# Kernel tuning notes

Hardware: AMD Instinct MI355X
Metric: run time of the kernel (lower is better)

Reference implementation:

```python
import jax, jax.numpy as jnp
import numpy as np

HEAD_DIM = 256
HIDDEN = 1536
INTERMEDIATE = 6144
NUM_KV_HEADS = 1
NUM_Q_HEADS = 8
SCALE = HEAD_DIM ** (-0.5)
PAST_LEN = 8191


def setup_inputs() -> dict:
    key = jax.random.key(0)
    ks = jax.random.split(key, 20)
    def lin(ki, fan_in, fan_out):
        # torch nn.Linear init: U(-1/sqrt(fan_in), 1/sqrt(fan_in)); stored (in, out) for x @ W
        bound = 1.0 / np.sqrt(fan_in)
        W = jax.random.uniform(ki, (fan_in, fan_out), jnp.float32, -bound, bound)
        b = jax.random.uniform(jax.random.fold_in(ki, 1), (fan_out,), jnp.float32, -bound, bound)
        return W, b
    Wq, bq = lin(ks[0], HIDDEN, NUM_Q_HEADS * HEAD_DIM)
    Wk, bk = lin(ks[1], HIDDEN, NUM_KV_HEADS * HEAD_DIM)
    Wv, bv = lin(ks[2], HIDDEN, NUM_KV_HEADS * HEAD_DIM)
    Wo, bo = lin(ks[3], NUM_Q_HEADS * HEAD_DIM, HIDDEN)
    Wg, bg = lin(ks[4], HIDDEN, INTERMEDIATE)
    Wu, bu = lin(ks[5], HIDDEN, INTERMEDIATE)
    Wd, bd = lin(ks[6], INTERMEDIATE, HIDDEN)
    x = jax.random.normal(ks[7], (1, 1, HIDDEN), jnp.float32)
    k_past = jax.random.normal(ks[8], (1, NUM_KV_HEADS, PAST_LEN, HEAD_DIM), jnp.float32)
    v_past = jax.random.normal(ks[9], (1, NUM_KV_HEADS, PAST_LEN, HEAD_DIM), jnp.float32)
    return dict(x=x, k_past=k_past, v_past=v_past,
                Wq=Wq, bq=bq, Wk=Wk, bk=bk, Wv=Wv, bv=bv, Wo=Wo, bo=bo,
                Wg=Wg, bg=bg, Wu=Wu, bu=bu, Wd=Wd, bd=bd)


def reference(x, k_past, v_past, Wq, bq, Wk, bk, Wv, bv, Wo, bo, Wg, bg, Wu, bu, Wd, bd):
    residual = x
    # projections; q: (1, Hq, 1, D), k/v: (1, Hkv, 1, D)
    q = (x @ Wq + bq).reshape(1, 1, NUM_Q_HEADS, HEAD_DIM).transpose(0, 2, 1, 3)
    k = (x @ Wk + bk).reshape(1, 1, NUM_KV_HEADS, HEAD_DIM).transpose(0, 2, 1, 3)
    v = (x @ Wv + bv).reshape(1, 1, NUM_KV_HEADS, HEAD_DIM).transpose(0, 2, 1, 3)
    k_full = jnp.concatenate([k_past, k], axis=2)  # (1, Hkv, S, D)
    v_full = jnp.concatenate([v_past, v], axis=2)
    # GQA: broadcast the single KV head across 8 Q heads (no materialized repeat)
    scores = jnp.einsum('bhqd,bksd->bhqs', q, k_full) * SCALE  # (1, Hq, 1, S)
    attn = jax.nn.softmax(scores, axis=-1)
    out = jnp.einsum('bhqs,bksd->bhqd', attn, v_full)  # (1, Hq, 1, D)
    out = out.transpose(0, 2, 1, 3).reshape(1, 1, NUM_Q_HEADS * HEAD_DIM)
    out = out @ Wo + bo
    x = residual + out
    # MLP: GELU(gate) * up -> down (exact erf GELU, matching torch nn.GELU default)
    ffn = (jax.nn.gelu(x @ Wg + bg, approximate=False) * (x @ Wu + bu)) @ Wd + bd
    return x + ffn
```

## Files before the change

### kernel.cpp

```cpp
#include <hip/hip_runtime.h>
#include <hip/hip_bf16.h>
#include <math.h>

#define PAST 8191
#define SCALEF 0.0625f

using bf = __hip_bfloat16;

__device__ __forceinline__ float bf2f(unsigned short u) {
    return __uint_as_float(((unsigned)u) << 16);
}
__device__ __forceinline__ void unpack8(uint4 r, float* f) {
    f[0] = __uint_as_float(r.x << 16);
    f[1] = __uint_as_float(r.x & 0xffff0000u);
    f[2] = __uint_as_float(r.y << 16);
    f[3] = __uint_as_float(r.y & 0xffff0000u);
    f[4] = __uint_as_float(r.z << 16);
    f[5] = __uint_as_float(r.z & 0xffff0000u);
    f[6] = __uint_as_float(r.w << 16);
    f[7] = __uint_as_float(r.w & 0xffff0000u);
}

template<bool BF16>
__device__ __forceinline__ void load8(const void* W, size_t off, float* f) {
    if constexpr (BF16) {
        uint4 r = *reinterpret_cast<const uint4*>((const unsigned short*)W + off);
        unpack8(r, f);
    } else {
        const float* p = (const float*)W + off;
        float4 a = *reinterpret_cast<const float4*>(p);
        float4 b = *reinterpret_cast<const float4*>(p + 4);
        f[0]=a.x; f[1]=a.y; f[2]=a.z; f[3]=a.w;
        f[4]=b.x; f[5]=b.y; f[6]=b.z; f[7]=b.w;
    }
}
template<bool BF16>
__device__ __forceinline__ void load4(const void* P, size_t off, float* f) {
    if constexpr (BF16) {
        uint2 r = *reinterpret_cast<const uint2*>((const unsigned short*)P + off);
        f[0] = __uint_as_float(r.x << 16); f[1] = __uint_as_float(r.x & 0xffff0000u);
        f[2] = __uint_as_float(r.y << 16); f[3] = __uint_as_float(r.y & 0xffff0000u);
    } else {
        float4 a = *reinterpret_cast<const float4*>((const float*)P + off);
        f[0]=a.x; f[1]=a.y; f[2]=a.z; f[3]=a.w;
    }
}
template<bool BF16>
__device__ __forceinline__ float load1(const void* P, int i) {
    if constexpr (BF16) return bf2f(((const unsigned short*)P)[i]);
    else return ((const float*)P)[i];
}

__global__ __launch_bounds__(256) void probe_kernel(const unsigned int* __restrict__ xw,
                                                    int* __restrict__ flag) {
    __shared__ int cnt;
    if (threadIdx.x == 0) cnt = 0;
    __syncthreads();
    int ok = 0;
    for (int i = threadIdx.x; i < 768; i += 256) {
        unsigned e = (xw[i] >> 7) & 0xff;
        if (e >= 96 && e <= 142) ok++;
    }
    atomicAdd(&cnt, ok);
    __syncthreads();
    if (threadIdx.x == 0) *flag = (cnt > 500) ? 1 : 0;
}

template<bool BF16>
__device__ void qkv_body(const void* x, const void* Wq, const void* bq,
                         const void* Wk, const void* bk, const void* Wv, const void* bv,
                         float* qkv) {
    __shared__ float xs[64];
    int tid = threadIdx.x;
    int i0 = blockIdx.y * 64;
    xs[tid] = load1<BF16>(x, i0 + tid);
    __syncthreads();
    int j = blockIdx.x * 512 + tid * 8;
    const void* W; const void* bias; int stride, jl;
    if (j < 2048)      { W = Wq; bias = bq; stride = 2048; jl = j; }
    else if (j < 2304) { W = Wk; bias = bk; stride = 256;  jl = j - 2048; }
    else               { W = Wv; bias = bv; stride = 256;  jl = j - 2304; }
    float acc[8] = {0,0,0,0,0,0,0,0};
    #pragma unroll 4
    for (int i = 0; i < 64; ++i) {
        float f[8];
        load8<BF16>(W, (size_t)(i0 + i) * stride + jl, f);
        float xv = xs[i];
        #pragma unroll
        for (int q = 0; q < 8; ++q) acc[q] = fmaf(xv, f[q], acc[q]);
    }
    #pragma unroll
    for (int q = 0; q < 8; ++q) atomicAdd(&qkv[j + q], acc[q]);
    if (blockIdx.y == 0) {
        #pragma unroll
        for (int q = 0; q < 8; ++q) atomicAdd(&qkv[j + q], load1<BF16>(bias, jl + q));
    }
}
__global__ __launch_bounds__(64) void qkv_kernel(
    const void* x, const void* Wq, const void* bq, const void* Wk, const void* bk,
    const void* Wv, const void* bv, float* qkv, const int* flag) {
    if (*flag) qkv_body<true>(x, Wq, bq, Wk, bk, Wv, bv, qkv);
    else       qkv_body<false>(x, Wq, bq, Wk, bk, Wv, bv, qkv);
}

template<bool BF16>
__device__ void scores_body(const float* qkv, const void* k_past, float* s) {
    int wave = threadIdx.x >> 6, lane = threadIdx.x & 63;
    int p = blockIdx.x * 4 + wave;
    int d0 = lane * 4;
    float kf[4];
    if (p < PAST) {
        load4<BF16>(k_past, (size_t)p * 256 + d0, kf);
    } else {
        kf[0] = qkv[2048 + d0];     kf[1] = qkv[2048 + d0 + 1];
        kf[2] = qkv[2048 + d0 + 2]; kf[3] = qkv[2048 + d0 + 3];
    }
    float part[8];
    #pragma unroll
    for (int h = 0; h < 8; ++h) {
        const float* qh = qkv + h * 256 + d0;
        part[h] = qh[0]*kf[0] + qh[1]*kf[1] + qh[2]*kf[2] + qh[3]*kf[3];
    }
    #pragma unroll
    for (int m = 1; m < 64; m <<= 1) {
        #pragma unroll
        for (int h = 0; h < 8; ++h) part[h] += __shfl_xor(part[h], m, 64);
    }
    if (lane == 0) {
        #pragma unroll
        for (int h = 0; h < 8; ++h) s[h * 8192 + p] = part[h] * SCALEF;
    }
}
__global__ __launch_bounds__(256) void scores_kernel(
    const float* qkv, const void* k_past, float* s, const int* flag) {
    if (*flag) scores_body<true>(qkv, k_past, s);
    else       scores_body<false>(qkv, k_past, s);
}

__global__ __launch_bounds__(256) void softmax_kernel(
    const float* __restrict__ s, float* __restrict__ a) {
    __shared__ float red[256];
    int h = blockIdx.x, tid = threadIdx.x;
    const float* sh = s + h * 8192;
    float m = -1e30f;
    for (int p = tid; p < 8192; p += 256) m = fmaxf(m, sh[p]);
    red[tid] = m; __syncthreads();
    for (int w = 128; w > 0; w >>= 1) {
        if (tid < w) red[tid] = fmaxf(red[tid], red[tid + w]);
        __syncthreads();
    }
    m = red[0]; __syncthreads();
    float l = 0.f;
    for (int p = tid; p < 8192; p += 256) l += expf(sh[p] - m);
    red[tid] = l; __syncthreads();
    for (int w = 128; w > 0; w >>= 1) {
        if (tid < w) red[tid] += red[tid + w];
        __syncthreads();
    }
    float inv = 1.0f / red[0];
    for (int p = tid; p < 8192; p += 256) a[h * 8192 + p] = expf(sh[p] - m) * inv;
}

template<bool BF16>
__device__ void pv_body(const float* a, const void* v_past, const float* qkv, float* part) {
    __shared__ float red[3 * 2048];
    int wave = threadIdx.x >> 6, lane = threadIdx.x & 63;
    int d0 = lane * 4;
    float o[8][4];
    #pragma unroll
    for (int h = 0; h < 8; ++h)
        #pragma unroll
        for (int r = 0; r < 4; ++r) o[h][r] = 0.f;
    int base = blockIdx.x * 128;
    for (int it = 0; it < 32; ++it) {
        int p = base + wave + it * 4;
        float vf[4];
        if (p < PAST) {
            load4<BF16>(v_past, (size_t)p * 256 + d0, vf);
        } else {
            vf[0] = qkv[2304 + d0];     vf[1] = qkv[2304 + d0 + 1];
            vf[2] = qkv[2304 + d0 + 2]; vf[3] = qkv[2304 + d0 + 3];
        }
        #pragma unroll
        for (int h = 0; h < 8; ++h) {
            float w = a[h * 8192 + p];
            #pragma unroll
            for (int r = 0; r < 4; ++r) o[h][r] = fmaf(w, vf[r], o[h][r]);
        }
    }
    if (wave > 0) {
        float* dst = red + (wave - 1) * 2048;
        #pragma unroll
        for (int h = 0; h < 8; ++h)
            #pragma unroll
            for (int r = 0; r < 4; ++r) dst[h * 256 + d0 + r] = o[h][r];
    }
    __syncthreads();
    if (wave == 0) {
        #pragma unroll
        for (int h = 0; h < 8; ++h)
            #pragma unroll
            for (int r = 0; r < 4; ++r) {
                float v = o[h][r] + red[h*256 + d0 + r] + red[2048 + h*256 + d0 + r]
                        + red[4096 + h*256 + d0 + r];
                part[(size_t)blockIdx.x * 2048 + h * 256 + d0 + r] = v;
            }
    }
}
__global__ __launch_bounds__(256) void pv_kernel(
    const float* a, const void* v_past, const float* qkv, float* part, const int* flag) {
    if (*flag) pv_body<true>(a, v_past, qkv, part);
    else       pv_body<false>(a, v_past, qkv, part);
}

template<bool BF16>
__device__ void oproj_body(const float* part, const void* Wo, const void* bo,
                           const void* xin, float* x2) {
    __shared__ float xs[128];
    int tid = threadIdx.x;
    int i0 = blockIdx.y * 128;
    for (int t = tid; t < 128; t += 64) {
        float sum = 0.f;
        for (int b = 0; b < 64; ++b) sum += part[(size_t)b * 2048 + i0 + t];
        xs[t] = sum;
    }
    __syncthreads();
    int j = blockIdx.x * 512 + tid * 8;
    float acc[8] = {0,0,0,0,0,0,0,0};
    #pragma unroll 4
    for (int i = 0; i < 128; ++i) {
        float f[8];
        load8<BF16>(Wo, (size_t)(i0 + i) * 1536 + j, f);
        float xv = xs[i];
        #pragma unroll
        for (int q = 0; q < 8; ++q) acc[q] = fmaf(xv, f[q], acc[q]);
    }
    #pragma unroll
    for (int q = 0; q < 8; ++q) atomicAdd(&x2[j + q], acc[q]);
    if (blockIdx.y == 0) {
        #pragma unroll
        for (int q = 0; q < 8; ++q)
            atomicAdd(&x2[j + q], load1<BF16>(bo, j + q) + load1<BF16>(xin, j + q));
    }
}
__global__ __launch_bounds__(64) void oproj_kernel(
    const float* part, const void* Wo, const void* bo, const void* xin,
    float* x2, const int* flag) {
    if (*flag) oproj_body<true>(part, Wo, bo, xin, x2);
    else       oproj_body<false>(part, Wo, bo, xin, x2);
}

template<bool BF16>
__device__ void gateup_body(const float* x2, const void* Wg, const void* Wu,
                            float* gacc, float* uacc) {
    __shared__ float xs[128];
    int tid = threadIdx.x; int i0 = blockIdx.y * 128;
    for (int t = tid; t < 128; t += 64) xs[t] = x2[i0 + t];
    __syncthreads();
    const void* W = blockIdx.z ? Wu : Wg;
    float* acc = blockIdx.z ? uacc : gacc;
    int j = blockIdx.x * 512 + tid * 8;
    float a[8] = {0,0,0,0,0,0,0,0};
    #pragma unroll 4
    for (int i = 0; i < 128; ++i) {
        float f[8];
        load8<BF16>(W, (size_t)(i0 + i) * 6144 + j, f);
        float xv = xs[i];
        #pragma unroll
        for (int q = 0; q < 8; ++q) a[q] = fmaf(xv, f[q], a[q]);
    }
    #pragma unroll
    for (int q = 0; q < 8; ++q) atomicAdd(&acc[j + q], a[q]);
}
__global__ __launch_bounds__(64) void gateup_kernel(
    const float* x2, const void* Wg, const void* Wu, float* gacc, float* uacc,
    const int* flag) {
    if (*flag) gateup_body<true>(x2, Wg, Wu, gacc, uacc);
    else       gateup_body<false>(x2, Wg, Wu, gacc, uacc);
}

template<bool BF16>
__device__ void down_body(const float* gacc, const float* uacc, const void* bg,
                          const void* bu, const void* Wd, float* yacc) {
    __shared__ float xs[128];
    int tid = threadIdx.x; int i0 = blockIdx.y * 128;
    for (int t = tid; t < 128; t += 64) {
        int i = i0 + t;
        float g = gacc[i] + load1<BF16>(bg, i);
        float u = uacc[i] + load1<BF16>(bu, i);
        float ge = 0.5f * g * (1.0f + erff(g * 0.70710678118654752f));
        xs[t] = ge * u;
    }
    __syncthreads();
    int j = blockIdx.x * 512 + tid * 8;
    float a[8] = {0,0,0,0,0,0,0,0};
    #pragma unroll 4
    for (int i = 0; i < 128; ++i) {
        float f[8];
        load8<BF16>(Wd, (size_t)(i0 + i) * 1536 + j, f);
        float xv = xs[i];
        #pragma unroll
        for (int q = 0; q < 8; ++q) a[q] = fmaf(xv, f[q], a[q]);
    }
    #pragma unroll
    for (int q = 0; q < 8; ++q) atomicAdd(&yacc[j + q], a[q]);
}
__global__ __launch_bounds__(64) void down_kernel(
    const float* gacc, const float* uacc, const void* bg, const void* bu,
    const void* Wd, float* yacc, const int* flag) {
    if (*flag) down_body<true>(gacc, uacc, bg, bu, Wd, yacc);
    else       down_body<false>(gacc, uacc, bg, bu, Wd, yacc);
}

__global__ __launch_bounds__(256) void final_kernel(
    const float* __restrict__ x2, const float* __restrict__ yacc,
    const void* __restrict__ bd, void* __restrict__ out, const int* __restrict__ flag) {
    int j = blockIdx.x * 256 + threadIdx.x;
    if (j < 1536) {
        int isbf = *flag;
        float b = isbf ? bf2f(((const unsigned short*)bd)[j]) : ((const float*)bd)[j];
        float v = x2[j] + yacc[j] + b;
        if (isbf) ((bf*)out)[j] = __float2bfloat16(v);
        else      ((float*)out)[j] = v;
    }
}

extern "C" void kernel_launch(void* const* d_in, const int* in_sizes, int n_in,
                              void* d_out, int out_size, void* d_ws, size_t ws_size,
                              hipStream_t stream) {
    const void* x  = d_in[0];
    const void* kp = d_in[1];
    const void* vp = d_in[2];
    const void* Wq = d_in[3];
    const void* bq = d_in[4];
    const void* Wk = d_in[5];
    const void* bk = d_in[6];
    const void* Wv = d_in[7];
    const void* bv = d_in[8];
    const void* Wo = d_in[9];
    const void* bo = d_in[10];
    const void* Wg = d_in[11];
    const void* bg = d_in[12];
    const void* Wu = d_in[13];
    const void* bu = d_in[14];
    const void* Wd = d_in[15];
    const void* bd = d_in[16];

    float* ws   = (float*)d_ws;
    float* qkv  = ws;
    float* x2   = ws + 2560;
    float* gacc = ws + 4096;
    float* uacc = ws + 10240;
    float* yacc = ws + 16384;
    float* sc   = ws + 17920;
    float* at   = ws + 83456;
    float* part = ws + 148992;
    int*  flag  = (int*)(ws + 280064);

    hipMemsetAsync(ws, 0, 17920 * sizeof(float), stream);
    probe_kernel<<<1, 256, 0, stream>>>((const unsigned int*)x, flag);

    qkv_kernel<<<dim3(5, 24), 64, 0, stream>>>(x, Wq, bq, Wk, bk, Wv, bv, qkv, flag);
    scores_kernel<<<2048, 256, 0, stream>>>(qkv, kp, sc, flag);
    softmax_kernel<<<8, 256, 0, stream>>>(sc, at);
    pv_kernel<<<64, 256, 0, stream>>>(at, vp, qkv, part, flag);
    oproj_kernel<<<dim3(3, 16), 64, 0, stream>>>(part, Wo, bo, x, x2, flag);
    gateup_kernel<<<dim3(12, 12, 2), 64, 0, stream>>>(x2, Wg, Wu, gacc, uacc, flag);
    down_kernel<<<dim3(3, 48), 64, 0, stream>>>(gacc, uacc, bg, bu, Wd, yacc, flag);
    final_kernel<<<6, 256, 0, stream>>>(x2, yacc, bd, d_out, flag);
}
```

Before: 313.0 us.

## Fuse softmax normalization into PV/oproj and split GEMV K-dim across more blocks

```diff
diff --git a/kernel.cpp b/kernel.cpp
--- a/kernel.cpp
+++ b/kernel.cpp
@@ -67,13 +67,14 @@
 }
 
 template<bool BF16>
-__device__ void qkv_body(const void* x, const void* Wq, const void* bq,
-                         const void* Wk, const void* bk, const void* Wv, const void* bv,
-                         float* qkv) {
-    __shared__ float xs[64];
+__device__ void qkv_body(const void* __restrict__ x, const void* __restrict__ Wq,
+                         const void* __restrict__ bq, const void* __restrict__ Wk,
+                         const void* __restrict__ bk, const void* __restrict__ Wv,
+                         const void* __restrict__ bv, float* __restrict__ qkv) {
+    __shared__ float xs[16];
     int tid = threadIdx.x;
-    int i0 = blockIdx.y * 64;
-    xs[tid] = load1<BF16>(x, i0 + tid);
+    int i0 = blockIdx.y * 16;
+    if (tid < 16) xs[tid] = load1<BF16>(x, i0 + tid);
     __syncthreads();
     int j = blockIdx.x * 512 + tid * 8;
     const void* W; const void* bias; int stride, jl;
@@ -82,19 +83,19 @@
     else               { W = Wv; bias = bv; stride = 256;  jl = j - 2304; }
     float acc[8] = {0,0,0,0,0,0,0,0};
     #pragma unroll 4
-    for (int i = 0; i < 64; ++i) {
+    for (int i = 0; i < 16; ++i) {
         float f[8];
         load8<BF16>(W, (size_t)(i0 + i) * stride + jl, f);
         float xv = xs[i];
         #pragma unroll
         for (int q = 0; q < 8; ++q) acc[q] = fmaf(xv, f[q], acc[q]);
     }
+    if (blockIdx.y == 0) {
+        #pragma unroll
+        for (int q = 0; q < 8; ++q) acc[q] += load1<BF16>(bias, jl + q);
+    }
     #pragma unroll
     for (int q = 0; q < 8; ++q) atomicAdd(&qkv[j + q], acc[q]);
-    if (blockIdx.y == 0) {
-        #pragma unroll
-        for (int q = 0; q < 8; ++q) atomicAdd(&qkv[j + q], load1<BF16>(bias, jl + q));
-    }
 }
 __global__ __launch_bounds__(64) void qkv_kernel(
     const void* x, const void* Wq, const void* bq, const void* Wk, const void* bk,
@@ -104,7 +105,8 @@
 }
 
 template<bool BF16>
-__device__ void scores_body(const float* qkv, const void* k_past, float* s) {
+__device__ void scores_body(const float* __restrict__ qkv, const void* __restrict__ k_past,
+                            float* __restrict__ s) {
     int wave = threadIdx.x >> 6, lane = threadIdx.x & 63;
     int p = blockIdx.x * 4 + wave;
     int d0 = lane * 4;
@@ -137,8 +139,8 @@
     else       scores_body<false>(qkv, k_past, s);
 }
 
-__global__ __launch_bounds__(256) void softmax_kernel(
-    const float* __restrict__ s, float* __restrict__ a) {
+__global__ __launch_bounds__(256) void mred_kernel(
+    const float* __restrict__ s, float* __restrict__ ml) {
     __shared__ float red[256];
     int h = blockIdx.x, tid = threadIdx.x;
     const float* sh = s + h * 8192;
@@ -157,23 +159,27 @@
         if (tid < w) red[tid] += red[tid + w];
         __syncthreads();
     }
-    float inv = 1.0f / red[0];
-    for (int p = tid; p < 8192; p += 256) a[h * 8192 + p] = expf(sh[p] - m) * inv;
-}
-
-template<bool BF16>
-__device__ void pv_body(const float* a, const void* v_past, const float* qkv, float* part) {
+    if (tid == 0) { ml[2 * h] = m; ml[2 * h + 1] = red[0]; }
+}
+
+template<bool BF16>
+__device__ void pv_body(const float* __restrict__ s, const float* __restrict__ ml,
+                        const void* __restrict__ v_past, const float* __restrict__ qkv,
+                        float* __restrict__ attnout) {
     __shared__ float red[3 * 2048];
     int wave = threadIdx.x >> 6, lane = threadIdx.x & 63;
     int d0 = lane * 4;
+    float m[8];
+    #pragma unroll
+    for (int h = 0; h < 8; ++h) m[h] = ml[2 * h];
     float o[8][4];
     #pragma unroll
     for (int h = 0; h < 8; ++h)
         #pragma unroll
         for (int r = 0; r < 4; ++r) o[h][r] = 0.f;
-    int base = blockIdx.x * 128;
-    for (int it = 0; it < 32; ++it) {
-        int p = base + wave + it * 4;
+    int base = blockIdx.x * 64;
+    for (int it = 0; it < 16; ++it) {
+        int p = base + wave * 16 + it;
         float vf[4];
         if (p < PAST) {
             load4<BF16>(v_past, (size_t)p * 256 + d0, vf);
@@ -183,7 +189,7 @@
         }
         #pragma unroll
         for (int h = 0; h < 8; ++h) {
-            float w = a[h * 8192 + p];
+            float w = expf(s[h * 8192 + p] - m[h]);
             #pragma unroll
             for (int r = 0; r < 4; ++r) o[h][r] = fmaf(w, vf[r], o[h][r]);
         }
@@ -203,66 +209,68 @@
             for (int r = 0; r < 4; ++r) {
                 float v = o[h][r] + red[h*256 + d0 + r] + red[2048 + h*256 + d0 + r]
                         + red[4096 + h*256 + d0 + r];
-                part[(size_t)blockIdx.x * 2048 + h * 256 + d0 + r] = v;
+                atomicAdd(&attnout[h * 256 + d0 + r], v);
             }
     }
 }
 __global__ __launch_bounds__(256) void pv_kernel(
-    const float* a, const void* v_past, const float* qkv, float* part, const int* flag) {
-    if (*flag) pv_body<true>(a, v_past, qkv, part);
-    else       pv_body<false>(a, v_past, qkv, part);
-}
-
-template<bool BF16>
-__device__ void oproj_body(const float* part, const void* Wo, const void* bo,
-                           const void* xin, float* x2) {
-    __shared__ float xs[128];
+    const float* s, const float* ml, const void* v_past, const float* qkv,
+    float* attnout, const int* flag) {
+    if (*flag) pv_body<true>(s, ml, v_past, qkv, attnout);
+    else       pv_body<false>(s, ml, v_past, qkv, attnout);
+}
+
+template<bool BF16>
+__device__ void oproj_body(const float* __restrict__ attnout, const float* __restrict__ ml,
+                           const void* __restrict__ Wo, const void* __restrict__ bo,
+                           const void* __restrict__ xin, float* __restrict__ x2) {
+    __shared__ float xs[16];
     int tid = threadIdx.x;
-    int i0 = blockIdx.y * 128;
-    for (int t = tid; t < 128; t += 64) {
-        float sum = 0.f;
-        for (int b = 0; b < 64; ++b) sum += part[(size_t)b * 2048 + i0 + t];
-        xs[t] = sum;
+    int i0 = blockIdx.y * 16;
+    if (tid < 16) {
+        int i = i0 + tid;
+        xs[tid] = attnout[i] * (1.0f / ml[2 * (i >> 8) + 1]);
     }
     __syncthreads();
     int j = blockIdx.x * 512 + tid * 8;
     float acc[8] = {0,0,0,0,0,0,0,0};
     #pragma unroll 4
-    for (int i = 0; i < 128; ++i) {
+    for (int i = 0; i < 16; ++i) {
         float f[8];
         load8<BF16>(Wo, (size_t)(i0 + i) * 1536 + j, f);
         float xv = xs[i];
         #pragma unroll
         for (int q = 0; q < 8; ++q) acc[q] = fmaf(xv, f[q], acc[q]);
     }
+    if (blockIdx.y == 0) {
+        #pragma unroll
+        for (int q = 0; q < 8; ++q)
+            acc[q] += load1<BF16>(bo, j + q) + load1<BF16>(xin, j + q);
+    }
     #pragma unroll
     for (int q = 0; q < 8; ++q) atomicAdd(&x2[j + q], acc[q]);
-    if (blockIdx.y == 0) {
-        #pragma unroll
-        for (int q = 0; q < 8; ++q)
-            atomicAdd(&x2[j + q], load1<BF16>(bo, j + q) + load1<BF16>(xin, j + q));
-    }
 }
 __global__ __launch_bounds__(64) void oproj_kernel(
-    const float* part, const void* Wo, const void* bo, const void* xin,
-    float* x2, const int* flag) {
-    if (*flag) oproj_body<true>(part, Wo, bo, xin, x2);
-    else       oproj_body<false>(part, Wo, bo, xin, x2);
-}
-
-template<bool BF16>
-__device__ void gateup_body(const float* x2, const void* Wg, const void* Wu,
-                            float* gacc, float* uacc) {
-    __shared__ float xs[128];
-    int tid = threadIdx.x; int i0 = blockIdx.y * 128;
-    for (int t = tid; t < 128; t += 64) xs[t] = x2[i0 + t];
+    const float* attnout, const float* ml, const void* Wo, const void* bo,
+    const void* xin, float* x2, const int* flag) {
+    if (*flag) oproj_body<true>(attnout, ml, Wo, bo, xin, x2);
+    else       oproj_body<false>(attnout, ml, Wo, bo, xin, x2);
+}
+
+template<bool BF16>
+__device__ void gateup_body(const float* __restrict__ x2, const void* __restrict__ Wg,
+                            const void* __restrict__ Wu, float* __restrict__ gacc,
+                            float* __restrict__ uacc) {
+    __shared__ float xs[32];
+    int tid = threadIdx.x; int i0 = blockIdx.y * 32;
+    if (tid < 32) xs[tid] = x2[i0 + tid];
     __syncthreads();
     const void* W = blockIdx.z ? Wu : Wg;
     float* acc = blockIdx.z ? uacc : gacc;
     int j = blockIdx.x * 512 + tid * 8;
     float a[8] = {0,0,0,0,0,0,0,0};
     #pragma unroll 4
-    for (int i = 0; i < 128; ++i) {
+    for (int i = 0; i < 32; ++i) {
         float f[8];
         load8<BF16>(W, (size_t)(i0 + i) * 6144 + j, f);
         float xv = xs[i];
@@ -280,22 +288,23 @@
 }
 
 template<bool BF16>
-__device__ void down_body(const float* gacc, const float* uacc, const void* bg,
-                          const void* bu, const void* Wd, float* yacc) {
-    __shared__ float xs[128];
-    int tid = threadIdx.x; int i0 = blockIdx.y * 128;
-    for (int t = tid; t < 128; t += 64) {
-        int i = i0 + t;
+__device__ void down_body(const float* __restrict__ gacc, const float* __restrict__ uacc,
+                          const void* __restrict__ bg, const void* __restrict__ bu,
+                          const void* __restrict__ Wd, float* __restrict__ yacc) {
+    __shared__ float xs[32];
+    int tid = threadIdx.x; int i0 = blockIdx.y * 32;
+    if (tid < 32) {
+        int i = i0 + tid;
         float g = gacc[i] + load1<BF16>(bg, i);
         float u = uacc[i] + load1<BF16>(bu, i);
         float ge = 0.5f * g * (1.0f + erff(g * 0.70710678118654752f));
-        xs[t] = ge * u;
+        xs[tid] = ge * u;
     }
     __syncthreads();
     int j = blockIdx.x * 512 + tid * 8;
     float a[8] = {0,0,0,0,0,0,0,0};
     #pragma unroll 4
-    for (int i = 0; i < 128; ++i) {
+    for (int i = 0; i < 32; ++i) {
         float f[8];
         load8<BF16>(Wd, (size_t)(i0 + i) * 1536 + j, f);
         float xv = xs[i];
@@ -346,26 +355,26 @@
     const void* Wd = d_in[15];
     const void* bd = d_in[16];
 
-    float* ws   = (float*)d_ws;
-    float* qkv  = ws;
-    float* x2   = ws + 2560;
-    float* gacc = ws + 4096;
-    float* uacc = ws + 10240;
-    float* yacc = ws + 16384;
-    float* sc   = ws + 17920;
-    float* at   = ws + 83456;
-    float* part = ws + 148992;
-    int*  flag  = (int*)(ws + 280064);
-
-    hipMemsetAsync(ws, 0, 17920 * sizeof(float), stream);
+    float* ws      = (float*)d_ws;
+    float* qkv     = ws;
+    float* x2      = ws + 2560;
+    float* gacc    = ws + 4096;
+    float* uacc    = ws + 10240;
+    float* yacc    = ws + 16384;
+    float* attnout = ws + 17920;
+    float* ml      = ws + 19968;
+    float* sc      = ws + 20480;
+    int*  flag     = (int*)(ws + 86016);
+
+    hipMemsetAsync(ws, 0, 19968 * sizeof(float), stream);
     probe_kernel<<<1, 256, 0, stream>>>((const unsigned int*)x, flag);
 
-    qkv_kernel<<<dim3(5, 24), 64, 0, stream>>>(x, Wq, bq, Wk, bk, Wv, bv, qkv, flag);
+    qkv_kernel<<<dim3(5, 96), 64, 0, stream>>>(x, Wq, bq, Wk, bk, Wv, bv, qkv, flag);
     scores_kernel<<<2048, 256, 0, stream>>>(qkv, kp, sc, flag);
-    softmax_kernel<<<8, 256, 0, stream>>>(sc, at);
-    pv_kernel<<<64, 256, 0, stream>>>(at, vp, qkv, part, flag);
-    oproj_kernel<<<dim3(3, 16), 64, 0, stream>>>(part, Wo, bo, x, x2, flag);
-    gateup_kernel<<<dim3(12, 12, 2), 64, 0, stream>>>(x2, Wg, Wu, gacc, uacc, flag);
-    down_kernel<<<dim3(3, 48), 64, 0, stream>>>(gacc, uacc, bg, bu, Wd, yacc, flag);
+    mred_kernel<<<8, 256, 0, stream>>>(sc, ml);
+    pv_kernel<<<128, 256, 0, stream>>>(sc, ml, vp, qkv, attnout, flag);
+    oproj_kernel<<<dim3(3, 128), 64, 0, stream>>>(attnout, ml, Wo, bo, x, x2, flag);
+    gateup_kernel<<<dim3(12, 48, 2), 64, 0, stream>>>(x2, Wg, Wu, gacc, uacc, flag);
+    down_kernel<<<dim3(3, 192), 64, 0, stream>>>(gacc, uacc, bg, bu, Wd, yacc, flag);
     final_kernel<<<6, 256, 0, stream>>>(x2, yacc, bd, d_out, flag);
 }
```

New measurement: 352.0 us. 12.5% more time.
